# Kernel tuning notes

Measured on AMD Instinct MI355X. Metric: run time of the kernel, lower is better.

The kernel has to match this reference:

```python
import jax, jax.numpy as jnp
import numpy as np

HIDDEN = 512
STATE = 256
DT = 0.1
LN_EPS = 1e-5


def setup_inputs() -> dict:
    key = jax.random.key(0)
    ks = jax.random.split(key, 9)
    B, T = 128, 256
    x = jax.random.normal(ks[0], (B, T, HIDDEN), dtype=jnp.float32)
    A = jax.random.normal(ks[1], (STATE, STATE), dtype=jnp.float32) * 0.01
    # nn.Linear default init scale ~ 1/sqrt(fan_in); exact dist irrelevant for a baseline
    Wb = jax.random.normal(ks[2], (STATE, HIDDEN), dtype=jnp.float32) / np.sqrt(HIDDEN)
    bb = jax.random.normal(ks[3], (STATE,), dtype=jnp.float32) * 0.01
    Wc = jax.random.normal(ks[4], (HIDDEN, STATE), dtype=jnp.float32) / np.sqrt(STATE)
    bc = jax.random.normal(ks[5], (HIDDEN,), dtype=jnp.float32) * 0.01
    Wd = jax.random.normal(ks[6], (HIDDEN, HIDDEN), dtype=jnp.float32) / np.sqrt(HIDDEN)
    bd = jax.random.normal(ks[7], (HIDDEN,), dtype=jnp.float32) * 0.01
    gamma = jnp.ones((HIDDEN,), dtype=jnp.float32)
    beta = jnp.zeros((HIDDEN,), dtype=jnp.float32)
    return {"x": x, "A": A, "Wb": Wb, "bb": bb, "Wc": Wc, "bc": bc,
            "Wd": Wd, "bd": bd, "gamma": gamma, "beta": beta}


def reference(x, A, Wb, bb, Wc, bc, Wd, bd, gamma, beta):
    B, T, H = x.shape
    # discrete transition via matrix exponential (torch.matrix_exp equivalent)
    Ad = jax.scipy.linalg.expm(A * DT)  # [S, S]
    # precompute input injection B(x_t) for all timesteps: [B, T, S]
    Bx = jnp.einsum('bth,sh->bts', x, Wb) + bb
    # linear recurrence h_t = h_{t-1} @ Ad^T + Bx_t via scan over time
    def step(h, bx_t):
        h = h @ Ad.T + bx_t  # [B, S]
        return h, h
    h0 = jnp.zeros((B, STATE), dtype=x.dtype)
    _, hs = jax.lax.scan(step, h0, jnp.swapaxes(Bx, 0, 1))  # hs: [T, B, S]
    hs = jnp.swapaxes(hs, 0, 1)  # [B, T, S]
    # y_t = C(h_t) + D(x_t), vectorized over time
    y = jnp.einsum('bts,hs->bth', hs, Wc) + bc \
        + jnp.einsum('bth,gh->btg', x, Wd) + bd
    # residual + layer norm (dropout is identity in eval mode)
    out = y + x
    mu = jnp.mean(out, axis=-1, keepdims=True)
    var = jnp.var(out, axis=-1, keepdims=True)
    return (out - mu) * jax.lax.rsqrt(var + LN_EPS) * gamma + beta
```

## Files before the change

kernel.cpp:

```cpp
#include <hip/hip_runtime.h>

#define HID 512
#define ST  256
#define BB  128
#define TT  256
#define BT  (BB*TT)
#define NCH 8
#define CHL 32

typedef unsigned short u16;
typedef unsigned int   u32;
typedef float f32x4  __attribute__((ext_vector_type(4)));
typedef __bf16 bf16x8 __attribute__((ext_vector_type(8)));

#define OFF_E    0x0u
#define OFF_EL   0x20000u
#define OFF_W32  0x40000u
#define OFF_WB   0x80000u
#define OFF_WCD  0xC0000u
#define OFF_BIAS 0x180000u
#define OFF_R    0x182000u
#define OFF_HC   0x282000u
#define OFF_MH   0x390000u
#define OFF_ML   0x3B0000u
#define OFF_U    0x400000u
#define OFF_HS   0x1400000u
#define OFF_XB   0x2400000u

__device__ __forceinline__ u16 f2bf(float f){
  u32 x = __float_as_uint(f);
  return (u16)((x + 0x7FFFu + ((x>>16)&1u)) >> 16);
}
__device__ __forceinline__ float bf2f(u16 u){
  return __uint_as_float(((u32)u)<<16);
}
__device__ __forceinline__ void gld16(const void* g, void* l){
  __builtin_amdgcn_global_load_lds((const __attribute__((address_space(1))) u32*)g,
                                   (__attribute__((address_space(3))) u32*)l, 16, 0, 0);
}

__global__ __launch_bounds__(256) void k_pe(
    const float* __restrict__ x, const float* __restrict__ A,
    const float* __restrict__ Wb, const float* __restrict__ Wc,
    const float* __restrict__ Wd, const float* __restrict__ bc,
    const float* __restrict__ bd, u16* __restrict__ Mhi,
    u16* __restrict__ Mlo, u16* __restrict__ wbb,
    u16* __restrict__ wcdb, float* __restrict__ biascd,
    u16* __restrict__ xb)
{
  long gt = (long)blockIdx.x*256 + threadIdx.x;
  const long np = 2048l*256l;
  for (long i = gt; i < (long)BT*HID/4; i += np){
    float4 v = ((const float4*)x)[i];
    u32 lo = (u32)f2bf(v.x) | ((u32)f2bf(v.y)<<16);
    u32 hi = (u32)f2bf(v.z) | ((u32)f2bf(v.w)<<16);
    uint2 q; q.x = lo; q.y = hi;
    ((uint2*)xb)[i] = q;
  }
  for (long i = gt; i < (long)ST*HID; i += np) wbb[i] = f2bf(Wb[i]);
  for (long i = gt; i < 512l*256l; i += np)
    wcdb[(size_t)(i>>8)*768 + (i&255)] = f2bf(Wc[i]);
  for (long i = gt; i < 512l*512l; i += np)
    wcdb[(size_t)(i>>9)*768 + 256 + (i&511)] = f2bf(Wd[i]);
  for (long i = gt; i < 256l*256l; i += np){
    float m = A[i]*0.1f;
    u16 h = f2bf(m);
    Mhi[i] = h;
    Mlo[i] = f2bf(m - bf2f(h));
  }
  for (long i = gt; i < 512; i += np) biascd[i] = bc[i] + bd[i];
}

__global__ __launch_bounds__(256,1) void k_expm(
    const float* __restrict__ A, const u16* __restrict__ Mhi,
    const u16* __restrict__ Mlo, u16* __restrict__ Ebf,
    u16* __restrict__ Elo)
{
  __shared__ u16 V1h[16*256], V1l[16*256], V2h[16*256];
  int bn = blockIdx.x;
  int tid = threadIdx.x, lane = tid&63, w = tid>>6, l15 = lane&15, lg = lane>>4;
  int j = bn*16 + l15;
  float v1[4][4];
  #pragma unroll
  for (int mi=0;mi<4;++mi)
    #pragma unroll
    for (int r=0;r<4;++r){
      int i = w*64 + mi*16 + lg*4 + r;
      float v = 0.1f * A[(size_t)i*256 + j];
      v1[mi][r] = v;
      u16 h = f2bf(v);
      int off = (l15*512 + i*2) ^ ((l15&7)<<4);
      V1h[off>>1] = h;
      V1l[off>>1] = f2bf(v - bf2f(h));
    }
  __syncthreads();
  f32x4 a2[4] = {};
  #pragma unroll
  for (int kk=0;kk<8;++kk){
    int boff = (l15*512 + (kk*32 + lg*8)*2) ^ ((l15&7)<<4);
    bf16x8 bh = *(const bf16x8*)(V1h + (boff>>1));
    bf16x8 bl = *(const bf16x8*)(V1l + (boff>>1));
    #pragma unroll
    for (int mi=0;mi<4;++mi){
      size_t ro = (size_t)(w*64 + mi*16 + l15)*256 + kk*32 + lg*8;
      bf16x8 ah = *(const bf16x8*)(Mhi + ro);
      bf16x8 al = *(const bf16x8*)(Mlo + ro);
      a2[mi] = __builtin_amdgcn_mfma_f32_16x16x32_bf16(ah, bh, a2[mi],0,0,0);
      a2[mi] = __builtin_amdgcn_mfma_f32_16x16x32_bf16(ah, bl, a2[mi],0,0,0);
      a2[mi] = __builtin_amdgcn_mfma_f32_16x16x32_bf16(al, bh, a2[mi],0,0,0);
    }
  }
  #pragma unroll
  for (int mi=0;mi<4;++mi)
    #pragma unroll
    for (int r=0;r<4;++r){
      int i = w*64 + mi*16 + lg*4 + r;
      int off = (l15*512 + i*2) ^ ((l15&7)<<4);
      V2h[off>>1] = f2bf(a2[mi][r]);
    }
  __syncthreads();
  f32x4 a3[4] = {};
  #pragma unroll
  for (int kk=0;kk<8;++kk){
    int boff = (l15*512 + (kk*32 + lg*8)*2) ^ ((l15&7)<<4);
    bf16x8 bh = *(const bf16x8*)(V2h + (boff>>1));
    #pragma unroll
    for (int mi=0;mi<4;++mi){
      bf16x8 ah = *(const bf16x8*)(Mhi + (size_t)(w*64 + mi*16 + l15)*256 + kk*32 + lg*8);
      a3[mi] = __builtin_amdgcn_mfma_f32_16x16x32_bf16(ah, bh, a3[mi],0,0,0);
    }
  }
  #pragma unroll
  for (int mi=0;mi<4;++mi)
    #pragma unroll
    for (int r=0;r<4;++r){
      int i = w*64 + mi*16 + lg*4 + r;
      float s = v1[mi][r] + 0.5f*a2[mi][r] + (1.f/6.f)*a3[mi][r];
      u16 h = f2bf(s);
      Ebf[(size_t)i*256 + j] = h;
      Elo[(size_t)i*256 + j] = f2bf(s - bf2f(h));
    }
}

__global__ __launch_bounds__(256,1) void k_bx(
    const u16* __restrict__ xb, const u16* __restrict__ wb,
    const float* __restrict__ bb, u16* __restrict__ uout)
{
  __shared__ u16 At[2][128*32];
  __shared__ u16 Bt[2][128*32];
  int bid = blockIdx.x;
  int m0 = (bid>>1)*128, n0 = (bid&1)*128;
  int tid = threadIdx.x, lane = tid&63, w = tid>>6, l15 = lane&15, lg = lane>>4;
  int wrow = (w>>1)*64, wcol = (w&1)*64;
  f32x4 acc[4][4] = {};

  auto stage = [&](int buf, int ki){
    #pragma unroll
    for (int p=0;p<2;++p){
      int c = w + p*4;
      int grow = c*16 + (lane>>2);
      int gk = ki*32 + (lane&3)*8;
      gld16(xb + (size_t)(m0+grow)*HID + gk, &At[buf][c*512]);
      gld16(wb + (size_t)(n0+grow)*HID + gk, &Bt[buf][c*512]);
    }
  };
  stage(0,0);
  __syncthreads();
  for (int ki=0; ki<16; ++ki){
    int buf = ki&1;
    if (ki < 15) stage(buf^1, ki+1);
    bf16x8 af[4], bfr[4];
    #pragma unroll
    for (int mi=0;mi<4;++mi)
      af[mi] = *(const bf16x8*)&At[buf][(wrow + mi*16 + l15)*32 + lg*8];
    #pragma unroll
    for (int ni=0;ni<4;++ni)
      bfr[ni] = *(const bf16x8*)&Bt[buf][(wcol + ni*16 + l15)*32 + lg*8];
    #pragma unroll
    for (int mi=0;mi<4;++mi)
      #pragma unroll
      for (int ni=0;ni<4;++ni)
        acc[mi][ni] = __builtin_amdgcn_mfma_f32_16x16x32_bf16(af[mi], bfr[ni], acc[mi][ni], 0,0,0);
    __syncthreads();
  }
  float bb4[4];
  #pragma unroll
  for (int ni=0;ni<4;++ni) bb4[ni] = bb[n0 + wcol + ni*16 + l15];
  #pragma unroll
  for (int mi=0;mi<4;++mi)
    #pragma unroll
    for (int ni=0;ni<4;++ni)
      #pragma unroll
      for (int r=0;r<4;++r){
        int row = m0 + wrow + mi*16 + lg*4 + r;
        int col = n0 + wcol + ni*16 + l15;
        uout[(size_t)row*ST + col] = f2bf(acc[mi][ni][r] + bb4[ni]);
      }
}

template<bool WRITE_HS>
__global__ __launch_bounds__(256,1) void k_rec(
    const u16* __restrict__ Ebf, const u16* __restrict__ Elo,
    const u16* __restrict__ ubuf, const float* __restrict__ Hc,
    float* __restrict__ Rbuf, u16* __restrict__ hsb,
    float* __restrict__ W32)
{
  int tid = threadIdx.x, lane = tid&63, w = tid>>6, l15 = lane&15, lg = lane>>4;
  __shared__ u16 hlds[2][16*256];

  if (!WRITE_HS && blockIdx.x >= 64){
    int b0 = ((int)blockIdx.x - 64)*16;
    bf16x8 ef[4][8], ef2[4][8];
    #pragma unroll
    for (int nt=0; nt<4; ++nt){
      int srow = w*64 + nt*16 + l15;
      #pragma unroll
      for (int kk=0; kk<8; ++kk){
        ef [nt][kk] = *(const bf16x8*)(Ebf + (size_t)srow*256 + kk*32 + lg*8);
        ef2[nt][kk] = *(const bf16x8*)(Elo + (size_t)srow*256 + kk*32 + lg*8);
      }
    }
    f32x4 acc[4];
    #pragma unroll
    for (int nt=0;nt<4;++nt)
      #pragma unroll
      for (int r=0;r<4;++r)
        acc[nt][r] = (b0 + lg*4 + r == w*64 + nt*16 + l15) ? 1.f : 0.f;
    for (int it=0; it<CHL; ++it){
      u16* hb = hlds[it&1];
      #pragma unroll
      for (int nt=0;nt<4;++nt)
        #pragma unroll
        for (int r=0;r<4;++r){
          int row = lg*4 + r;
          int sc  = w*64 + nt*16 + l15;
          int off = (row*512 + sc*2) ^ ((row&7)<<4);
          hb[off>>1] = f2bf(acc[nt][r]);
        }
      __syncthreads();
      bf16x8 af[8];
      #pragma unroll
      for (int kk=0;kk<8;++kk){
        int off = (l15*512 + (kk*32 + lg*8)*2) ^ ((l15&7)<<4);
        af[kk] = *(const bf16x8*)(hb + (off>>1));
      }
      #pragma unroll
      for (int nt=0;nt<4;++nt)
        #pragma unroll
        for (int kk=0;kk<8;++kk)
          acc[nt] = __builtin_amdgcn_mfma_f32_16x16x32_bf16(af[kk], ef[nt][kk], acc[nt], 0,0,0);
      #pragma unroll
      for (int nt=0;nt<4;++nt)
        #pragma unroll
        for (int kk=0;kk<8;++kk)
          acc[nt] = __builtin_amdgcn_mfma_f32_16x16x32_bf16(af[kk], ef2[nt][kk], acc[nt], 0,0,0);
    }
    #pragma unroll
    for (int nt=0;nt<4;++nt)
      #pragma unroll
      for (int r=0;r<4;++r)
        W32[(size_t)(b0 + lg*4 + r)*256 + w*64 + nt*16 + l15] = acc[nt][r];
    return;
  }

  int j = (int)blockIdx.x >> 3;
  int b0 = ((int)blockIdx.x & 7)*16;

  bf16x8 ef[4][8];
  #pragma unroll
  for (int nt=0; nt<4; ++nt){
    int srow = w*64 + nt*16 + l15;
    #pragma unroll
    for (int kk=0; kk<8; ++kk)
      ef[nt][kk] = *(const bf16x8*)(Ebf + (size_t)srow*256 + kk*32 + lg*8);
  }

  f32x4 acc[4];
  #pragma unroll
  for (int nt=0;nt<4;++nt){
    if (WRITE_HS && j > 0){
      #pragma unroll
      for (int r=0;r<4;++r)
        acc[nt][r] = Hc[((size_t)j*BB + b0 + lg*4 + r)*ST + w*64 + nt*16 + l15];
    } else {
      acc[nt] = (f32x4){0.f,0.f,0.f,0.f};
    }
  }

  int t0 = j*CHL;
  float uv[4][4];
  #pragma unroll
  for (int nt=0;nt<4;++nt)
    #pragma unroll
    for (int r=0;r<4;++r)
      uv[nt][r] = bf2f(ubuf[((size_t)(b0 + lg*4 + r)*TT + t0)*ST + w*64 + nt*16 + l15]);

  for (int it=0; it<CHL; ++it){
    int t = t0 + it;
    u16* hb = hlds[it&1];
    #pragma unroll
    for (int nt=0;nt<4;++nt)
      #pragma unroll
      for (int r=0;r<4;++r){
        int row = lg*4 + r;
        int sc  = w*64 + nt*16 + l15;
        int off = (row*512 + sc*2) ^ ((row&7)<<4);
        hb[off>>1] = f2bf(acc[nt][r]);
      }
    __syncthreads();
    float uvn[4][4];
    if (it+1 < CHL){
      #pragma unroll
      for (int nt=0;nt<4;++nt)
        #pragma unroll
        for (int r=0;r<4;++r)
          uvn[nt][r] = bf2f(ubuf[((size_t)(b0 + lg*4 + r)*TT + t + 1)*ST + w*64 + nt*16 + l15]);
    }
    bf16x8 af[8];
    #pragma unroll
    for (int kk=0;kk<8;++kk){
      int off = (l15*512 + (kk*32 + lg*8)*2) ^ ((l15&7)<<4);
      af[kk] = *(const bf16x8*)(hb + (off>>1));
    }
    #pragma unroll
    for (int nt=0;nt<4;++nt)
      #pragma unroll
      for (int kk=0;kk<8;++kk)
        acc[nt] = __builtin_amdgcn_mfma_f32_16x16x32_bf16(af[kk], ef[nt][kk], acc[nt], 0,0,0);
    #pragma unroll
    for (int nt=0;nt<4;++nt)
      #pragma unroll
      for (int r=0;r<4;++r)
        acc[nt][r] += uv[nt][r];
    if (WRITE_HS){
      #pragma unroll
      for (int nt=0;nt<4;++nt)
        #pragma unroll
        for (int r=0;r<4;++r)
          hsb[((size_t)(b0 + lg*4 + r)*TT + t)*ST + w*64 + nt*16 + l15] = f2bf(acc[nt][r]);
    }
    if (it+1 < CHL){
      #pragma unroll
      for (int nt=0;nt<4;++nt)
        #pragma unroll
        for (int r=0;r<4;++r)
          uv[nt][r] = uvn[nt][r];
    }
  }
  if (!WRITE_HS){
    #pragma unroll
    for (int nt=0;nt<4;++nt)
      #pragma unroll
      for (int r=0;r<4;++r)
        Rbuf[((size_t)j*BB + b0 + lg*4 + r)*ST + w*64 + nt*16 + l15] = acc[nt][r];
  }
}

__global__ __launch_bounds__(256) void k_scan(
    const float* __restrict__ W32, const float* __restrict__ Rbuf,
    float* __restrict__ Hc)
{
  int b = blockIdx.x;
  int s = threadIdx.x;
  __shared__ float hp[256];
  float h = Rbuf[(size_t)(0*BB + b)*ST + s];
  Hc[(size_t)(1*BB + b)*ST + s] = h;
  for (int j = 2; j < NCH; ++j){
    hp[s] = h;
    __syncthreads();
    float a = Rbuf[(size_t)((j-1)*BB + b)*ST + s];
    #pragma unroll 4
    for (int k=0;k<256;++k)
      a = fmaf(hp[k], W32[(size_t)k*256 + s], a);
    __syncthreads();
    h = a;
    Hc[(size_t)j*BB*ST + (size_t)b*ST + s] = h;
  }
}

__global__ __launch_bounds__(512,2) void k_out(
    const u16* __restrict__ hsb, const u16* __restrict__ xb,
    const u16* __restrict__ wcd, const float* __restrict__ biascd,
    const float* __restrict__ gamma, const float* __restrict__ beta,
    float* __restrict__ out)
{
  __shared__ u16 At[2][64*32];
  __shared__ u16 Bt[2][512*32];
  __shared__ float redbuf[64][8][2];
  __shared__ float musig[64][2];
  int m0 = blockIdx.x*64;
  int tid = threadIdx.x, lane = tid&63, w = tid>>6, l15 = lane&15, lg = lane>>4;
  f32x4 acc[4][4] = {};

  auto stage = [&](int buf, int ki){
    #pragma unroll
    for (int p=0;p<4;++p){
      int c = w + p*8;
      gld16(wcd + (size_t)(c*16 + (lane>>2))*768 + ki*32 + (lane&3)*8, &Bt[buf][c*512]);
    }
    if (w < 4){
      const u16* g;
      if (ki < 8) g = hsb + (size_t)(m0 + w*16 + (lane>>2))*ST  + ki*32 + (lane&3)*8;
      else        g = xb  + (size_t)(m0 + w*16 + (lane>>2))*HID + (ki-8)*32 + (lane&3)*8;
      gld16(g, &At[buf][w*512]);
    }
  };
  stage(0,0);
  __syncthreads();
  for (int ki=0; ki<24; ++ki){
    int buf = ki&1;
    if (ki < 23) stage(buf^1, ki+1);
    bf16x8 af[4], bfr[4];
    #pragma unroll
    for (int mi=0;mi<4;++mi)
      af[mi] = *(const bf16x8*)&At[buf][(mi*16 + l15)*32 + lg*8];
    #pragma unroll
    for (int ni=0;ni<4;++ni)
      bfr[ni] = *(const bf16x8*)&Bt[buf][(w*64 + ni*16 + l15)*32 + lg*8];
    #pragma unroll
    for (int mi=0;mi<4;++mi)
      #pragma unroll
      for (int ni=0;ni<4;++ni)
        acc[mi][ni] = __builtin_amdgcn_mfma_f32_16x16x32_bf16(af[mi], bfr[ni], acc[mi][ni], 0,0,0);
    __syncthreads();
  }
  float g4[4], b4[4], bias4[4];
  #pragma unroll
  for (int ni=0;ni<4;++ni){
    int col = w*64 + ni*16 + l15;
    g4[ni] = gamma[col]; b4[ni] = beta[col]; bias4[ni] = biascd[col];
  }
  float psum[4][4] = {}, psq[4][4] = {};
  #pragma unroll
  for (int mi=0;mi<4;++mi)
    #pragma unroll
    for (int ni=0;ni<4;++ni)
      #pragma unroll
      for (int r=0;r<4;++r){
        int row = m0 + mi*16 + lg*4 + r;
        int col = w*64 + ni*16 + l15;
        float v = acc[mi][ni][r] + bias4[ni] + bf2f(xb[(size_t)row*HID + col]);
        acc[mi][ni][r] = v;
        psum[mi][r] += v; psq[mi][r] += v*v;
      }
  #pragma unroll
  for (int mi=0;mi<4;++mi)
    #pragma unroll
    for (int r=0;r<4;++r)
      #pragma unroll
      for (int d=1; d<16; d<<=1){
        psum[mi][r] += __shfl_xor(psum[mi][r], d);
        psq[mi][r]  += __shfl_xor(psq[mi][r], d);
      }
  if (l15 == 0){
    #pragma unroll
    for (int mi=0;mi<4;++mi)
      #pragma unroll
      for (int r=0;r<4;++r){
        int rl = mi*16 + lg*4 + r;
        redbuf[rl][w][0] = psum[mi][r];
        redbuf[rl][w][1] = psq[mi][r];
      }
  }
  __syncthreads();
  if (tid < 64){
    float s=0.f, q=0.f;
    #pragma unroll
    for (int wv=0; wv<8; ++wv){ s += redbuf[tid][wv][0]; q += redbuf[tid][wv][1]; }
    float mu = s*(1.f/512.f);
    float var = q*(1.f/512.f) - mu*mu;
    musig[tid][0] = mu;
    musig[tid][1] = rsqrtf(var + 1e-5f);
  }
  __syncthreads();
  #pragma unroll
  for (int mi=0;mi<4;++mi)
    #pragma unroll
    for (int r=0;r<4;++r){
      int rl = mi*16 + lg*4 + r;
      float mu = musig[rl][0], rs = musig[rl][1];
      #pragma unroll
      for (int ni=0;ni<4;++ni){
        int col = w*64 + ni*16 + l15;
        out[(size_t)(m0+rl)*HID + col] = (acc[mi][ni][r] - mu)*rs*g4[ni] + b4[ni];
      }
    }
}

extern "C" void kernel_launch(void* const* d_in, const int* in_sizes, int n_in,
                              void* d_out, int out_size, void* d_ws, size_t ws_size,
                              hipStream_t stream)
{
  const float* x     = (const float*)d_in[0];
  const float* A     = (const float*)d_in[1];
  const float* Wb    = (const float*)d_in[2];
  const float* bb    = (const float*)d_in[3];
  const float* Wc    = (const float*)d_in[4];
  const float* bc    = (const float*)d_in[5];
  const float* Wd    = (const float*)d_in[6];
  const float* bd    = (const float*)d_in[7];
  const float* gamma = (const float*)d_in[8];
  const float* beta  = (const float*)d_in[9];

  char* ws = (char*)d_ws;
  u16*   Ebf    = (u16*)  (ws + OFF_E);
  u16*   Elo    = (u16*)  (ws + OFF_EL);
  float* W32    = (float*)(ws + OFF_W32);
  u16*   wbb    = (u16*)  (ws + OFF_WB);
  u16*   wcdb   = (u16*)  (ws + OFF_WCD);
  float* biascd = (float*)(ws + OFF_BIAS);
  float* Rbuf   = (float*)(ws + OFF_R);
  float* Hc     = (float*)(ws + OFF_HC);
  u16*   Mhi    = (u16*)  (ws + OFF_MH);
  u16*   Mlo    = (u16*)  (ws + OFF_ML);
  u16*   ubuf   = (u16*)  (ws + OFF_U);
  u16*   hsb    = (u16*)  (ws + OFF_HS);
  u16*   xb     = (u16*)  (ws + OFF_XB);

  k_pe<<<2048, 256, 0, stream>>>(x, A, Wb, Wc, Wd, bc, bd, Mhi, Mlo, wbb, wcdb, biascd, xb);
  k_expm<<<16, 256, 0, stream>>>(A, Mhi, Mlo, Ebf, Elo);
  k_bx<<<512, 256, 0, stream>>>(xb, wbb, bb, ubuf);
  k_rec<false><<<80, 256, 0, stream>>>(Ebf, Elo, ubuf, nullptr, Rbuf, nullptr, W32);
  k_scan<<<128, 256, 0, stream>>>(W32, Rbuf, Hc);
  k_rec<true><<<64, 256, 0, stream>>>(Ebf, Elo, ubuf, Hc, nullptr, hsb, W32);
  k_out<<<512, 512, 0, stream>>>(hsb, xb, wcdb, biascd, gamma, beta, (float*)d_out);
}
```

Measured before the change: 348.0 us.

## Use 16 shorter chunks with an MFMA inter-chunk scan and larger output tiles

The time recurrence is split into 16 chunks of 16 steps instead of 8 of 32, which doubles the number of blocks that run the serial chunk recurrence. The old scalar fp32 scan across chunks becomes a tensor-core scan that uses split-bf16 (hi/lo) copies of E^16 - I, updating chunk carries in place in Rbuf. The output GEMM+LayerNorm kernel moves to 1024-thread blocks covering 128 rows. The aim is to shorten the serial critical path and use more CUs. In exchange the scan runs more serial chunk steps, and split-bf16 may lose some precision.

New measurement: 330.0 us. 5.2% less time.

```diff
diff --git a/kernel.cpp b/kernel.cpp
--- a/kernel.cpp
+++ b/kernel.cpp
@@ -5,8 +5,8 @@
 #define BB  128
 #define TT  256
 #define BT  (BB*TT)
-#define NCH 8
-#define CHL 32
+#define NCH 16
+#define CHL 16
 
 typedef unsigned short u16;
 typedef unsigned int   u32;
@@ -15,14 +15,14 @@
 
 #define OFF_E    0x0u
 #define OFF_EL   0x20000u
-#define OFF_W32  0x40000u
+#define OFF_E16H 0x40000u
+#define OFF_E16L 0x60000u
 #define OFF_WB   0x80000u
 #define OFF_WCD  0xC0000u
 #define OFF_BIAS 0x180000u
-#define OFF_R    0x182000u
-#define OFF_HC   0x282000u
-#define OFF_MH   0x390000u
-#define OFF_ML   0x3B0000u
+#define OFF_MH   0x190000u
+#define OFF_ML   0x1B0000u
+#define OFF_R    0x200000u
 #define OFF_U    0x400000u
 #define OFF_HS   0x1400000u
 #define OFF_XB   0x2400000u
@@ -201,15 +201,15 @@
 template<bool WRITE_HS>
 __global__ __launch_bounds__(256,1) void k_rec(
     const u16* __restrict__ Ebf, const u16* __restrict__ Elo,
-    const u16* __restrict__ ubuf, const float* __restrict__ Hc,
-    float* __restrict__ Rbuf, u16* __restrict__ hsb,
-    float* __restrict__ W32)
+    const u16* __restrict__ ubuf, float* __restrict__ Rbuf,
+    u16* __restrict__ hsb, u16* __restrict__ E16h,
+    u16* __restrict__ E16l)
 {
   int tid = threadIdx.x, lane = tid&63, w = tid>>6, l15 = lane&15, lg = lane>>4;
   __shared__ u16 hlds[2][16*256];
 
-  if (!WRITE_HS && blockIdx.x >= 64){
-    int b0 = ((int)blockIdx.x - 64)*16;
+  if (!WRITE_HS && blockIdx.x >= 128){
+    int b0 = ((int)blockIdx.x - 128)*16;
     bf16x8 ef[4][8], ef2[4][8];
     #pragma unroll
     for (int nt=0; nt<4; ++nt){
@@ -242,7 +242,7 @@
       #pragma unroll
       for (int kk=0;kk<8;++kk){
         int off = (l15*512 + (kk*32 + lg*8)*2) ^ ((l15&7)<<4);
-        af[kk] = *(const bf16x8*)(hb + (off>>1));
+        af[kk] = *(const bf16x8*)(hlds[it&1] + (off>>1));
       }
       #pragma unroll
       for (int nt=0;nt<4;++nt)
@@ -258,8 +258,14 @@
     #pragma unroll
     for (int nt=0;nt<4;++nt)
       #pragma unroll
-      for (int r=0;r<4;++r)
-        W32[(size_t)(b0 + lg*4 + r)*256 + w*64 + nt*16 + l15] = acc[nt][r];
+      for (int r=0;r<4;++r){
+        int krow = b0 + lg*4 + r;
+        int col  = w*64 + nt*16 + l15;
+        float v = acc[nt][r] - ((krow == col) ? 1.f : 0.f);
+        u16 h = f2bf(v);
+        E16h[(size_t)col*256 + krow] = h;
+        E16l[(size_t)col*256 + krow] = f2bf(v - bf2f(h));
+      }
     return;
   }
 
@@ -281,7 +287,7 @@
     if (WRITE_HS && j > 0){
       #pragma unroll
       for (int r=0;r<4;++r)
-        acc[nt][r] = Hc[((size_t)j*BB + b0 + lg*4 + r)*ST + w*64 + nt*16 + l15];
+        acc[nt][r] = Rbuf[((size_t)(j-1)*BB + b0 + lg*4 + r)*ST + w*64 + nt*16 + l15];
     } else {
       acc[nt] = (f32x4){0.f,0.f,0.f,0.f};
     }
@@ -356,53 +362,108 @@
   }
 }
 
-__global__ __launch_bounds__(256) void k_scan(
-    const float* __restrict__ W32, const float* __restrict__ Rbuf,
-    float* __restrict__ Hc)
-{
-  int b = blockIdx.x;
-  int s = threadIdx.x;
-  __shared__ float hp[256];
-  float h = Rbuf[(size_t)(0*BB + b)*ST + s];
-  Hc[(size_t)(1*BB + b)*ST + s] = h;
-  for (int j = 2; j < NCH; ++j){
-    hp[s] = h;
+__global__ __launch_bounds__(256,1) void k_scan(
+    const u16* __restrict__ E16h, const u16* __restrict__ E16l,
+    float* __restrict__ Rbuf)
+{
+  int b0 = blockIdx.x*16;
+  int tid = threadIdx.x, lane = tid&63, w = tid>>6, l15 = lane&15, lg = lane>>4;
+  __shared__ u16 hh[2][16*256], hl[2][16*256];
+  bf16x8 efh[4][8], efl[4][8];
+  #pragma unroll
+  for (int nt=0; nt<4; ++nt){
+    int srow = w*64 + nt*16 + l15;
+    #pragma unroll
+    for (int kk=0; kk<8; ++kk){
+      efh[nt][kk] = *(const bf16x8*)(E16h + (size_t)srow*256 + kk*32 + lg*8);
+      efl[nt][kk] = *(const bf16x8*)(E16l + (size_t)srow*256 + kk*32 + lg*8);
+    }
+  }
+  int col[4], rowg[4];
+  #pragma unroll
+  for (int nt=0;nt<4;++nt) col[nt] = w*64 + nt*16 + l15;
+  #pragma unroll
+  for (int r=0;r<4;++r) rowg[r] = b0 + lg*4 + r;
+
+  f32x4 acc[4];
+  #pragma unroll
+  for (int nt=0;nt<4;++nt)
+    #pragma unroll
+    for (int r=0;r<4;++r)
+      acc[nt][r] = Rbuf[(size_t)rowg[r]*ST + col[nt]];
+
+  for (int j=2; j<NCH; ++j){
+    float rv[4][4];
+    #pragma unroll
+    for (int nt=0;nt<4;++nt)
+      #pragma unroll
+      for (int r=0;r<4;++r)
+        rv[nt][r] = Rbuf[((size_t)(j-1)*BB + rowg[r])*ST + col[nt]];
+    u16* bh = hh[j&1]; u16* bl = hl[j&1];
+    #pragma unroll
+    for (int nt=0;nt<4;++nt)
+      #pragma unroll
+      for (int r=0;r<4;++r){
+        int row = lg*4 + r;
+        int off = (row*512 + col[nt]*2) ^ ((row&7)<<4);
+        float v = acc[nt][r];
+        u16 h = f2bf(v);
+        bh[off>>1] = h;
+        bl[off>>1] = f2bf(v - bf2f(h));
+      }
     __syncthreads();
-    float a = Rbuf[(size_t)((j-1)*BB + b)*ST + s];
-    #pragma unroll 4
-    for (int k=0;k<256;++k)
-      a = fmaf(hp[k], W32[(size_t)k*256 + s], a);
-    __syncthreads();
-    h = a;
-    Hc[(size_t)j*BB*ST + (size_t)b*ST + s] = h;
-  }
-}
-
-__global__ __launch_bounds__(512,2) void k_out(
+    bf16x8 ah[8], al[8];
+    #pragma unroll
+    for (int kk=0;kk<8;++kk){
+      int off = (l15*512 + (kk*32 + lg*8)*2) ^ ((l15&7)<<4);
+      ah[kk] = *(const bf16x8*)(bh + (off>>1));
+      al[kk] = *(const bf16x8*)(bl + (off>>1));
+    }
+    #pragma unroll
+    for (int nt=0;nt<4;++nt)
+      #pragma unroll
+      for (int kk=0;kk<8;++kk){
+        acc[nt] = __builtin_amdgcn_mfma_f32_16x16x32_bf16(ah[kk], efh[nt][kk], acc[nt], 0,0,0);
+        acc[nt] = __builtin_amdgcn_mfma_f32_16x16x32_bf16(al[kk], efh[nt][kk], acc[nt], 0,0,0);
+        acc[nt] = __builtin_amdgcn_mfma_f32_16x16x32_bf16(ah[kk], efl[nt][kk], acc[nt], 0,0,0);
+      }
+    #pragma unroll
+    for (int nt=0;nt<4;++nt)
+      #pragma unroll
+      for (int r=0;r<4;++r){
+        acc[nt][r] += rv[nt][r];
+        Rbuf[((size_t)(j-1)*BB + rowg[r])*ST + col[nt]] = acc[nt][r];
+      }
+  }
+}
+
+__global__ __launch_bounds__(1024,4) void k_out(
     const u16* __restrict__ hsb, const u16* __restrict__ xb,
     const u16* __restrict__ wcd, const float* __restrict__ biascd,
     const float* __restrict__ gamma, const float* __restrict__ beta,
     float* __restrict__ out)
 {
-  __shared__ u16 At[2][64*32];
+  __shared__ u16 At[2][128*32];
   __shared__ u16 Bt[2][512*32];
-  __shared__ float redbuf[64][8][2];
-  __shared__ float musig[64][2];
-  int m0 = blockIdx.x*64;
-  int tid = threadIdx.x, lane = tid&63, w = tid>>6, l15 = lane&15, lg = lane>>4;
+  __shared__ float redbuf[128][8][2];
+  __shared__ float musig[128][2];
+  int m0 = blockIdx.x*128;
+  int tid = threadIdx.x, lane = tid&63, wid = tid>>6, l15 = lane&15, lg = lane>>4;
+  int wr = wid>>3, wc = wid&7;
   f32x4 acc[4][4] = {};
 
   auto stage = [&](int buf, int ki){
     #pragma unroll
-    for (int p=0;p<4;++p){
-      int c = w + p*8;
+    for (int p=0;p<2;++p){
+      int c = wid*2 + p;
       gld16(wcd + (size_t)(c*16 + (lane>>2))*768 + ki*32 + (lane&3)*8, &Bt[buf][c*512]);
     }
-    if (w < 4){
+    if (wid < 8){
+      int grow = m0 + wid*16 + (lane>>2);
       const u16* g;
-      if (ki < 8) g = hsb + (size_t)(m0 + w*16 + (lane>>2))*ST  + ki*32 + (lane&3)*8;
-      else        g = xb  + (size_t)(m0 + w*16 + (lane>>2))*HID + (ki-8)*32 + (lane&3)*8;
-      gld16(g, &At[buf][w*512]);
+      if (ki < 8) g = hsb + (size_t)grow*ST  + ki*32 + (lane&3)*8;
+      else        g = xb  + (size_t)grow*HID + (ki-8)*32 + (lane&3)*8;
+      gld16(g, &At[buf][wid*512]);
     }
   };
   stage(0,0);
@@ -413,10 +474,10 @@
     bf16x8 af[4], bfr[4];
     #pragma unroll
     for (int mi=0;mi<4;++mi)
-      af[mi] = *(const bf16x8*)&At[buf][(mi*16 + l15)*32 + lg*8];
+      af[mi] = *(const bf16x8*)&At[buf][(wr*64 + mi*16 + l15)*32 + lg*8];
     #pragma unroll
     for (int ni=0;ni<4;++ni)
-      bfr[ni] = *(const bf16x8*)&Bt[buf][(w*64 + ni*16 + l15)*32 + lg*8];
+      bfr[ni] = *(const bf16x8*)&Bt[buf][(wc*64 + ni*16 + l15)*32 + lg*8];
     #pragma unroll
     for (int mi=0;mi<4;++mi)
       #pragma unroll
@@ -427,8 +488,8 @@
   float g4[4], b4[4], bias4[4];
   #pragma unroll
   for (int ni=0;ni<4;++ni){
-    int col = w*64 + ni*16 + l15;
-    g4[ni] = gamma[col]; b4[ni] = beta[col]; bias4[ni] = biascd[col];
+    int c = wc*64 + ni*16 + l15;
+    g4[ni] = gamma[c]; b4[ni] = beta[c]; bias4[ni] = biascd[c];
   }
   float psum[4][4] = {}, psq[4][4] = {};
   #pragma unroll
@@ -437,9 +498,9 @@
     for (int ni=0;ni<4;++ni)
       #pragma unroll
       for (int r=0;r<4;++r){
-        int row = m0 + mi*16 + lg*4 + r;
-        int col = w*64 + ni*16 + l15;
-        float v = acc[mi][ni][r] + bias4[ni] + bf2f(xb[(size_t)row*HID + col]);
+        int row = m0 + wr*64 + mi*16 + lg*4 + r;
+        int c   = wc*64 + ni*16 + l15;
+        float v = acc[mi][ni][r] + bias4[ni] + bf2f(xb[(size_t)row*HID + c]);
         acc[mi][ni][r] = v;
         psum[mi][r] += v; psq[mi][r] += v*v;
       }
@@ -457,13 +518,13 @@
     for (int mi=0;mi<4;++mi)
       #pragma unroll
       for (int r=0;r<4;++r){
-        int rl = mi*16 + lg*4 + r;
-        redbuf[rl][w][0] = psum[mi][r];
-        redbuf[rl][w][1] = psq[mi][r];
+        int rl = wr*64 + mi*16 + lg*4 + r;
+        redbuf[rl][wc][0] = psum[mi][r];
+        redbuf[rl][wc][1] = psq[mi][r];
       }
   }
   __syncthreads();
-  if (tid < 64){
+  if (tid < 128){
     float s=0.f, q=0.f;
     #pragma unroll
     for (int wv=0; wv<8; ++wv){ s += redbuf[tid][wv][0]; q += redbuf[tid][wv][1]; }
@@ -477,12 +538,12 @@
   for (int mi=0;mi<4;++mi)
     #pragma unroll
     for (int r=0;r<4;++r){
-      int rl = mi*16 + lg*4 + r;
+      int rl = wr*64 + mi*16 + lg*4 + r;
       float mu = musig[rl][0], rs = musig[rl][1];
       #pragma unroll
       for (int ni=0;ni<4;++ni){
-        int col = w*64 + ni*16 + l15;
-        out[(size_t)(m0+rl)*HID + col] = (acc[mi][ni][r] - mu)*rs*g4[ni] + b4[ni];
+        int c = wc*64 + ni*16 + l15;
+        out[(size_t)(m0+rl)*HID + c] = (acc[mi][ni][r] - mu)*rs*g4[ni] + b4[ni];
       }
     }
 }
@@ -505,14 +566,14 @@
   char* ws = (char*)d_ws;
   u16*   Ebf    = (u16*)  (ws + OFF_E);
   u16*   Elo    = (u16*)  (ws + OFF_EL);
-  float* W32    = (float*)(ws + OFF_W32);
+  u16*   E16h   = (u16*)  (ws + OFF_E16H);
+  u16*   E16l   = (u16*)  (ws + OFF_E16L);
   u16*   wbb    = (u16*)  (ws + OFF_WB);
   u16*   wcdb   = (u16*)  (ws + OFF_WCD);
   float* biascd = (float*)(ws + OFF_BIAS);
-  float* Rbuf   = (float*)(ws + OFF_R);
-  float* Hc     = (float*)(ws + OFF_HC);
   u16*   Mhi    = (u16*)  (ws + OFF_MH);
   u16*   Mlo    = (u16*)  (ws + OFF_ML);
+  float* Rbuf   = (float*)(ws + OFF_R);
   u16*   ubuf   = (u16*)  (ws + OFF_U);
   u16*   hsb    = (u16*)  (ws + OFF_HS);
   u16*   xb     = (u16*)  (ws + OFF_XB);
@@ -520,8 +581,8 @@
   k_pe<<<2048, 256, 0, stream>>>(x, A, Wb, Wc, Wd, bc, bd, Mhi, Mlo, wbb, wcdb, biascd, xb);
   k_expm<<<16, 256, 0, stream>>>(A, Mhi, Mlo, Ebf, Elo);
   k_bx<<<512, 256, 0, stream>>>(xb, wbb, bb, ubuf);
-  k_rec<false><<<80, 256, 0, stream>>>(Ebf, Elo, ubuf, nullptr, Rbuf, nullptr, W32);
-  k_scan<<<128, 256, 0, stream>>>(W32, Rbuf, Hc);
-  k_rec<true><<<64, 256, 0, stream>>>(Ebf, Elo, ubuf, Hc, nullptr, hsb, W32);
-  k_out<<<512, 512, 0, stream>>>(hsb, xb, wcdb, biascd, gamma, beta, (float*)d_out);
-}
+  k_rec<false><<<144, 256, 0, stream>>>(Ebf, Elo, ubuf, Rbuf, nullptr, E16h, E16l);
+  k_scan<<<8, 256, 0, stream>>>(E16h, E16l, Rbuf);
+  k_rec<true><<<128, 256, 0, stream>>>(Ebf, Elo, ubuf, Rbuf, hsb, nullptr, nullptr);
+  k_out<<<256, 1024, 0, stream>>>(hsb, xb, wcdb, biascd, gamma, beta, (float*)d_out);
+}
```
